# Optimization experiments

Measured on AMD Instinct MI355X. Metric: run time of the kernel, lower is better.

Reference implementation:

```python
import jax, jax.numpy as jnp
import numpy as np

VOCAB = 400000
DIM = 300
NUM_QUERIES = 512
TOP_K = 5


def setup_inputs() -> dict:
    key = jax.random.key(0)
    k1, k2 = jax.random.split(key)
    embedding = jax.random.normal(k1, (VOCAB, DIM), dtype=jnp.float32)
    word_ids = jax.random.randint(k2, (NUM_QUERIES,), 0, VOCAB, dtype=jnp.int64)
    return {"embedding": embedding, "word_ids": word_ids, "k": TOP_K}


def reference(embedding, word_ids, k):
    # Row-normalize the table (done in Synonym.__init__: emb / emb.norm(dim=1, keepdim=True))
    E = embedding / jnp.linalg.norm(embedding, axis=1, keepdims=True)  # [V, d]
    # Per-word GEMV against the full table, batched over queries:
    # torch.mm(word_embedding.view(1,-1), embedding.t()) per word -> [Q, V]
    q = E[word_ids]                      # [Q, d] gather of query word vectors
    sims = jnp.einsum('qd,vd->qv', q, E)  # [Q, V] cosine similarities
    # topk(k, largest=True); the torch code sorts results by value afterwards,
    # lax.top_k already returns values in descending order.
    top_vals, top_ids = jax.lax.top_k(sims, k)  # [Q, k], [Q, k]
    return top_vals, top_ids
```

## Files before the change

### kernel.cpp

```cpp
#include <hip/hip_runtime.h>


#define VOCAB   400000
#define DIM     300
#define NQ      512
#define NT      25000
#define TILE_U  5120
#define QSTR    328
#define QFSTR   304
#define TOPK    5
#define NCAND   3072

using f32x4 = __attribute__((ext_vector_type(4))) float;
using s16x8 = __attribute__((ext_vector_type(8))) short;

__device__ __forceinline__ unsigned short f2bf(float f) {
  unsigned int u = __builtin_bit_cast(unsigned int, f);
  u += 0x7fffu + ((u >> 16) & 1u);
  return (unsigned short)(u >> 16);
}

__device__ __forceinline__ void ins3(float v, int id, float* tv, int* ti) {
  if (v > tv[2]) {
    if (v > tv[0]) {
      tv[2] = tv[1]; ti[2] = ti[1]; tv[1] = tv[0]; ti[1] = ti[0];
      tv[0] = v; ti[0] = id;
    } else if (v > tv[1]) {
      tv[2] = tv[1]; ti[2] = ti[1]; tv[1] = v; ti[1] = id;
    } else {
      tv[2] = v; ti[2] = id;
    }
  }
}

__global__ __launch_bounds__(64)
void qprep_kernel(const float* __restrict__ emb, const int* __restrict__ wid,
                  float* __restrict__ qf, unsigned short* __restrict__ qn) {
  const int q = blockIdx.x;
  const int lane = threadIdx.x;
  const long long w = (long long)wid[q];
  const float* row = emb + w * DIM;
  float x[5];
  double ss = 0.0;
#pragma unroll
  for (int j = 0; j < 5; ++j) {
    const int k = lane + 64 * j;
    x[j] = (k < DIM) ? row[k] : 0.0f;
    ss += (double)x[j] * (double)x[j];
  }
#pragma unroll
  for (int m = 1; m < 64; m <<= 1) ss += __shfl_xor(ss, m, 64);
  const double rinv = 1.0 / sqrt(ss);
#pragma unroll
  for (int j = 0; j < 5; ++j) {
    const int k = lane + 64 * j;
    if (k < DIM) {
      const float v = (float)((double)x[j] * rinv);
      qf[q * QFSTR + k] = v;
      qn[q * QSTR + k] = f2bf(v);
    }
  }
  if (lane < QSTR - DIM) qn[q * QSTR + DIM + lane] = 0;
}

__global__ __launch_bounds__(256)
void prenorm_kernel(const float* __restrict__ emb, unsigned short* __restrict__ sw) {
  const int wave = threadIdx.x >> 6, lane = threadIdx.x & 63;
  const int t = blockIdx.x * 4 + wave;
  const int r = lane & 15, grp = lane >> 4;
  const float* row = emb + (size_t)(t * 16 + r) * DIM;

  float x[10][8];
  float ss = 0.f;
#pragma unroll
  for (int ks = 0; ks < 10; ++ks) {
    const int k0 = ks * 32 + grp * 8;
    if (k0 + 8 <= DIM) {
      const f32x4 u = *(const f32x4*)(row + k0);
      const f32x4 v = *(const f32x4*)(row + k0 + 4);
#pragma unroll
      for (int j = 0; j < 4; ++j) { x[ks][j] = u[j]; x[ks][j + 4] = v[j]; }
    } else {
#pragma unroll
      for (int j = 0; j < 8; ++j) {
        const int k = k0 + j;
        x[ks][j] = (k < DIM) ? row[k] : 0.0f;
      }
    }
#pragma unroll
    for (int j = 0; j < 8; ++j) ss += x[ks][j] * x[ks][j];
  }
  ss += __shfl_xor(ss, 16, 64);
  ss += __shfl_xor(ss, 32, 64);
  const float rinv = rsqrtf(ss);

  unsigned short* dst = sw + (size_t)t * TILE_U + lane * 8;
#pragma unroll
  for (int ks = 0; ks < 10; ++ks) {
    uint4 pk;
    unsigned int w0 = f2bf(x[ks][0] * rinv) | ((unsigned int)f2bf(x[ks][1] * rinv) << 16);
    unsigned int w1 = f2bf(x[ks][2] * rinv) | ((unsigned int)f2bf(x[ks][3] * rinv) << 16);
    unsigned int w2 = f2bf(x[ks][4] * rinv) | ((unsigned int)f2bf(x[ks][5] * rinv) << 16);
    unsigned int w3 = f2bf(x[ks][6] * rinv) | ((unsigned int)f2bf(x[ks][7] * rinv) << 16);
    pk.x = w0; pk.y = w1; pk.z = w2; pk.w = w3;
    *(uint4*)(dst + ks * 512) = pk;
  }
}

__global__ __launch_bounds__(512, 2)
void score_kernel(const unsigned short* __restrict__ sw,
                  const unsigned short* __restrict__ qn,
                  float2* __restrict__ cand) {
  __shared__ __align__(16) unsigned short qlds[128 * QSTR];

  const int tid = threadIdx.x;
  const int wave = tid >> 6, lane = tid & 63;
  const int l15 = lane & 15, grp = lane >> 4;
  const int mtile = blockIdx.x & 3, rb = blockIdx.x >> 2;
  const int rowgrp = wave >> 1, qhalf = wave & 1;

  {
    const uint4* src = (const uint4*)(qn + (size_t)mtile * 128 * QSTR);
    uint4* dst = (uint4*)qlds;
    for (int i = tid; i < 128 * QSTR * 2 / 16; i += 512) dst[i] = src[i];
  }
  __syncthreads();

  float v3[4][3]; int i3[4][3];
#pragma unroll
  for (int qi = 0; qi < 4; ++qi)
#pragma unroll
    for (int j = 0; j < 3; ++j) { v3[qi][j] = -1e30f; i3[qi][j] = 0; }

  const s16x8 zz = {0, 0, 0, 0, 0, 0, 0, 0};
  const int qrow0 = qhalf * 64;

  for (int it = 0; it < 25; ++it) {
    const int tbase = it * 1024 + rb * 16 + rowgrp * 4;
    bool tv[4];
    const unsigned short* ap[4];
#pragma unroll
    for (int vi = 0; vi < 4; ++vi) {
      const int t = tbase + vi;
      tv[vi] = (t < NT);
      ap[vi] = sw + (size_t)(tv[vi] ? t : 0) * TILE_U + lane * 8;
    }

    f32x4 acc[4][4];
#pragma unroll
    for (int qi = 0; qi < 4; ++qi)
#pragma unroll
      for (int vi = 0; vi < 4; ++vi) acc[qi][vi] = {0.f, 0.f, 0.f, 0.f};

#pragma unroll
    for (int ks = 0; ks < 10; ++ks) {
      s16x8 a[4];
#pragma unroll
      for (int vi = 0; vi < 4; ++vi)
        a[vi] = tv[vi] ? *(const s16x8*)(ap[vi] + ks * 512) : zz;
      const unsigned short* bb = qlds + ks * 32 + grp * 8;
#pragma unroll
      for (int qi = 0; qi < 4; ++qi) {
        const s16x8 b = *(const s16x8*)(bb + (qrow0 + qi * 16 + l15) * QSTR);
#pragma unroll
        for (int vi = 0; vi < 4; ++vi)
          acc[qi][vi] = __builtin_amdgcn_mfma_f32_16x16x32_bf16(a[vi], b, acc[qi][vi], 0, 0, 0);
      }
    }

#pragma unroll
    for (int vi = 0; vi < 4; ++vi) {
      if (!tv[vi]) continue;
      const int rbase = (tbase + vi) * 16 + grp * 4;
#pragma unroll
      for (int qi = 0; qi < 4; ++qi) {
#pragma unroll
        for (int rr = 0; rr < 4; ++rr) {
          ins3(acc[qi][vi][rr], rbase + rr, &v3[qi][0], &i3[qi][0]);
        }
      }
    }
  }

  const int slotbase = rb * 48 + rowgrp * 12 + grp * 3;
#pragma unroll
  for (int qi = 0; qi < 4; ++qi) {
    const int q = mtile * 128 + qhalf * 64 + qi * 16 + l15;
    float2* dst = cand + (size_t)q * NCAND + slotbase;
#pragma unroll
    for (int j = 0; j < 3; ++j) {
      float2 e; e.x = v3[qi][j]; e.y = __int_as_float(i3[qi][j]);
      dst[j] = e;
    }
  }
}

__global__ __launch_bounds__(256)
void topk_kernel(const float* __restrict__ emb, const float* __restrict__ qf,
                 const float2* __restrict__ cand, float* __restrict__ out) {
  __shared__ float pV[256 * 6];
  __shared__ int   pI[256 * 6];
  __shared__ int   selI[32];
  __shared__ float resV[32];

  const int q = blockIdx.x;
  const int t = threadIdx.x;
  const float2* cq = cand + (size_t)q * NCAND;

  float bv[6]; int bi[6];
#pragma unroll
  for (int j = 0; j < 6; ++j) { bv[j] = -1e30f; bi[j] = -1; }
  for (int i = t; i < NCAND; i += 256) {
    const float2 e = cq[i];
    const float v = e.x;
    if (v > bv[5]) {
      bv[5] = v; bi[5] = __float_as_int(e.y);
#pragma unroll
      for (int j = 5; j > 0; --j) {
        if (bv[j] > bv[j - 1]) {
          const float tv2 = bv[j]; bv[j] = bv[j - 1]; bv[j - 1] = tv2;
          const int ti2 = bi[j]; bi[j] = bi[j - 1]; bi[j - 1] = ti2;
        }
      }
    }
  }
#pragma unroll
  for (int j = 0; j < 6; ++j) { pV[t * 6 + j] = bv[j]; pI[t * 6 + j] = bi[j]; }
  __syncthreads();

  if (t < 64) {
    for (int r = 0; r < 32; ++r) {
      float mv = -2e30f; int mp = 0;
      for (int i = t; i < 256 * 6; i += 64) {
        const float v = pV[i];
        if (v > mv) { mv = v; mp = i; }
      }
#pragma unroll
      for (int m = 1; m < 64; m <<= 1) {
        const float ov = __shfl_xor(mv, m, 64);
        const int   op = __shfl_xor(mp, m, 64);
        if (ov > mv) { mv = ov; mp = op; }
      }
      if (t == 0) { selI[r] = pI[mp]; pV[mp] = -2e30f; }
      __builtin_amdgcn_wave_barrier();
    }
  }
  __syncthreads();

  {
    const int j = t >> 3, sub = t & 7;
    const int id = selI[j];
    float dot = 0.f, sq = 0.f;
    if (id >= 0) {
      const f32x4* e4 = (const f32x4*)(emb + (size_t)id * DIM);
      const f32x4* q4 = (const f32x4*)(qf + (size_t)q * QFSTR);
      for (int f = sub; f < DIM / 4; f += 8) {
        const f32x4 ev = e4[f], qv = q4[f];
        dot += ev[0]*qv[0] + ev[1]*qv[1] + ev[2]*qv[2] + ev[3]*qv[3];
        sq  += ev[0]*ev[0] + ev[1]*ev[1] + ev[2]*ev[2] + ev[3]*ev[3];
      }
    }
#pragma unroll
    for (int m = 1; m < 8; m <<= 1) {
      dot += __shfl_xor(dot, m, 64);
      sq  += __shfl_xor(sq, m, 64);
    }
    if (sub == 0)
      resV[j] = (id >= 0 && sq > 0.f) ? (float)((double)dot / sqrt((double)sq)) : -2e30f;
  }
  __syncthreads();

  if (t == 0) {
#pragma unroll
    for (int r = 0; r < TOPK; ++r) {
      float mv = -3e30f; int mp = 0;
      for (int i = 0; i < 32; ++i) if (resV[i] > mv) { mv = resV[i]; mp = i; }
      out[q * TOPK + r] = mv;
      out[NQ * TOPK + q * TOPK + r] = (float)selI[mp];
      resV[mp] = -3e30f;
    }
  }
}

extern "C" void kernel_launch(void* const* d_in, const int* in_sizes, int n_in,
                              void* d_out, int out_size, void* d_ws, size_t ws_size,
                              hipStream_t stream) {
  (void)in_sizes; (void)n_in; (void)out_size; (void)ws_size;
  const float* emb = (const float*)d_in[0];
  const int* wid = (const int*)d_in[1];
  float* out = (float*)d_out;

  char* ws = (char*)d_ws;
  unsigned short* qn = (unsigned short*)ws;
  float*  qf   = (float*)(ws + 335872);
  float2* cand = (float2*)(ws + 958464);
  unsigned short* sw = (unsigned short*)(ws + 13541376);

  qprep_kernel<<<NQ, 64, 0, stream>>>(emb, wid, qf, qn);
  prenorm_kernel<<<NT / 4, 256, 0, stream>>>(emb, sw);
  score_kernel<<<256, 512, 0, stream>>>(sw, qn, cand);
  topk_kernel<<<NQ, 256, 0, stream>>>(emb, qf, cand, out);
}
```

Baseline: 1.088 ms.

## Restructure score kernel tiling with pre-swizzled query layout and early-skip top-3

Queries are now written by qprep in the same MFMA-swizzled bf16 tile layout as the table, so the score kernel loads B fragments from LDS with a conflict-free contiguous pattern. The score grid becomes 1024 blocks of 256 threads, each covering 64 queries, with smaller LDS and higher occupancy, and per-wave iteration counts that drop the bounds checks. The top-3 update is skipped when the max of four accumulator values cannot enter the list. A cross-lane shuffle merge reduces the four row-group lists to six candidates per wave. The cost is that the table stream is re-read by 8 query groups instead of 4, which doubles L2/HBM traffic for the embedding tiles.

```diff
diff --git a/kernel.cpp b/kernel.cpp
--- a/kernel.cpp
+++ b/kernel.cpp
@@ -6,7 +6,6 @@
 #define NQ      512
 #define NT      25000
 #define TILE_U  5120
-#define QSTR    328
 #define QFSTR   304
 #define TOPK    5
 #define NCAND   3072
@@ -35,7 +34,7 @@
 
 __global__ __launch_bounds__(64)
 void qprep_kernel(const float* __restrict__ emb, const int* __restrict__ wid,
-                  float* __restrict__ qf, unsigned short* __restrict__ qn) {
+                  float* __restrict__ qf, unsigned short* __restrict__ qsw) {
   const int q = blockIdx.x;
   const int lane = threadIdx.x;
   const long long w = (long long)wid[q];
@@ -54,13 +53,23 @@
 #pragma unroll
   for (int j = 0; j < 5; ++j) {
     const int k = lane + 64 * j;
-    if (k < DIM) {
-      const float v = (float)((double)x[j] * rinv);
-      qf[q * QFSTR + k] = v;
-      qn[q * QSTR + k] = f2bf(v);
-    }
-  }
-  if (lane < QSTR - DIM) qn[q * QSTR + DIM + lane] = 0;
+    if (k < DIM) qf[q * QFSTR + k] = (float)((double)x[j] * rinv);
+  }
+  if (lane < 40) {
+    const int ks = lane >> 2, grp = lane & 3;
+    const int k0 = ks * 32 + grp * 8;
+    unsigned int pw[4];
+#pragma unroll
+    for (int h = 0; h < 4; ++h) {
+      const int k = k0 + 2 * h;
+      float v0 = 0.f, v1 = 0.f;
+      if (k < DIM)     v0 = (float)((double)row[k] * rinv);
+      if (k + 1 < DIM) v1 = (float)((double)row[k + 1] * rinv);
+      pw[h] = (unsigned int)f2bf(v0) | ((unsigned int)f2bf(v1) << 16);
+    }
+    uint4 pk; pk.x = pw[0]; pk.y = pw[1]; pk.z = pw[2]; pk.w = pw[3];
+    *(uint4*)(qsw + (size_t)(q >> 4) * TILE_U + ks * 512 + grp * 128 + (q & 15) * 8) = pk;
+  }
 }
 
 __global__ __launch_bounds__(256)
@@ -107,22 +116,24 @@
   }
 }
 
-__global__ __launch_bounds__(512, 2)
+__global__ __launch_bounds__(256, 4)
 void score_kernel(const unsigned short* __restrict__ sw,
-                  const unsigned short* __restrict__ qn,
+                  const unsigned short* __restrict__ qsw,
                   float2* __restrict__ cand) {
-  __shared__ __align__(16) unsigned short qlds[128 * QSTR];
+  __shared__ __align__(16) unsigned short qlds[4 * TILE_U];
 
   const int tid = threadIdx.x;
   const int wave = tid >> 6, lane = tid & 63;
   const int l15 = lane & 15, grp = lane >> 4;
-  const int mtile = blockIdx.x & 3, rb = blockIdx.x >> 2;
-  const int rowgrp = wave >> 1, qhalf = wave & 1;
+  const int bid = blockIdx.x;
+  const int moct = (bid >> 3) & 7;
+  const int rb = (bid & 7) | ((bid >> 6) << 3);
 
   {
-    const uint4* src = (const uint4*)(qn + (size_t)mtile * 128 * QSTR);
+    const uint4* src = (const uint4*)(qsw + (size_t)moct * 4 * TILE_U);
     uint4* dst = (uint4*)qlds;
-    for (int i = tid; i < 128 * QSTR * 2 / 16; i += 512) dst[i] = src[i];
+#pragma unroll
+    for (int i = 0; i < 10; ++i) dst[tid + 256 * i] = src[tid + 256 * i];
   }
   __syncthreads();
 
@@ -132,19 +143,13 @@
 #pragma unroll
     for (int j = 0; j < 3; ++j) { v3[qi][j] = -1e30f; i3[qi][j] = 0; }
 
-  const s16x8 zz = {0, 0, 0, 0, 0, 0, 0, 0};
-  const int qrow0 = qhalf * 64;
-
-  for (int it = 0; it < 25; ++it) {
-    const int tbase = it * 1024 + rb * 16 + rowgrp * 4;
-    bool tv[4];
-    const unsigned short* ap[4];
-#pragma unroll
-    for (int vi = 0; vi < 4; ++vi) {
-      const int t = tbase + vi;
-      tv[vi] = (t < NT);
-      ap[vi] = sw + (size_t)(tv[vi] ? t : 0) * TILE_U + lane * 8;
-    }
+  const unsigned short* bq = qlds + lane * 8;
+  const int wt = rb * 16 + wave * 4;
+  const int nit = (wt < 424) ? 13 : 12;
+
+  for (int it = 0; it < nit; ++it) {
+    const int t0 = it * 2048 + wt;
+    const unsigned short* ap = sw + (size_t)t0 * TILE_U + lane * 8;
 
     f32x4 acc[4][4];
 #pragma unroll
@@ -157,11 +162,10 @@
       s16x8 a[4];
 #pragma unroll
       for (int vi = 0; vi < 4; ++vi)
-        a[vi] = tv[vi] ? *(const s16x8*)(ap[vi] + ks * 512) : zz;
-      const unsigned short* bb = qlds + ks * 32 + grp * 8;
+        a[vi] = *(const s16x8*)(ap + (size_t)vi * TILE_U + ks * 512);
 #pragma unroll
       for (int qi = 0; qi < 4; ++qi) {
-        const s16x8 b = *(const s16x8*)(bb + (qrow0 + qi * 16 + l15) * QSTR);
+        const s16x8 b = *(const s16x8*)(bq + qi * TILE_U + ks * 512);
 #pragma unroll
         for (int vi = 0; vi < 4; ++vi)
           acc[qi][vi] = __builtin_amdgcn_mfma_f32_16x16x32_bf16(a[vi], b, acc[qi][vi], 0, 0, 0);
@@ -170,27 +174,43 @@
 
 #pragma unroll
     for (int vi = 0; vi < 4; ++vi) {
-      if (!tv[vi]) continue;
-      const int rbase = (tbase + vi) * 16 + grp * 4;
+      const int rbase = (t0 + vi) * 16 + grp * 4;
 #pragma unroll
       for (int qi = 0; qi < 4; ++qi) {
-#pragma unroll
-        for (int rr = 0; rr < 4; ++rr) {
-          ins3(acc[qi][vi][rr], rbase + rr, &v3[qi][0], &i3[qi][0]);
+        const f32x4 a4 = acc[qi][vi];
+        const float m01 = fmaxf(a4[0], a4[1]);
+        const float m23 = fmaxf(a4[2], a4[3]);
+        if (fmaxf(m01, m23) > v3[qi][2]) {
+#pragma unroll
+          for (int rr = 0; rr < 4; ++rr)
+            ins3(a4[rr], rbase + rr, &v3[qi][0], &i3[qi][0]);
         }
       }
     }
   }
 
-  const int slotbase = rb * 48 + rowgrp * 12 + grp * 3;
 #pragma unroll
   for (int qi = 0; qi < 4; ++qi) {
-    const int q = mtile * 128 + qhalf * 64 + qi * 16 + l15;
-    float2* dst = cand + (size_t)q * NCAND + slotbase;
-#pragma unroll
-    for (int j = 0; j < 3; ++j) {
-      float2 e; e.x = v3[qi][j]; e.y = __int_as_float(i3[qi][j]);
-      dst[j] = e;
+    float m0 = v3[qi][0], m1 = v3[qi][1], m2 = v3[qi][2];
+    int   d0 = i3[qi][0], d1 = i3[qi][1], d2 = i3[qi][2];
+    const int q = moct * 64 + qi * 16 + l15;
+    float2* dst = cand + (size_t)q * NCAND + (rb * 24 + wave * 6);
+#pragma unroll
+    for (int r = 0; r < 6; ++r) {
+      float bv = m0; int bi = d0; int bl = grp;
+      float ov = __shfl_xor(bv, 16, 64);
+      int   oi = __shfl_xor(bi, 16, 64);
+      int   ol = __shfl_xor(bl, 16, 64);
+      if (ov > bv || (ov == bv && ol < bl)) { bv = ov; bi = oi; bl = ol; }
+      ov = __shfl_xor(bv, 32, 64);
+      oi = __shfl_xor(bi, 32, 64);
+      ol = __shfl_xor(bl, 32, 64);
+      if (ov > bv || (ov == bv && ol < bl)) { bv = ov; bi = oi; bl = ol; }
+      if (bl == grp) { m0 = m1; d0 = d1; m1 = m2; d1 = d2; m2 = -1e30f; }
+      if (r == grp || r == grp + 4) {
+        float2 e; e.x = bv; e.y = __int_as_float(bi);
+        dst[r] = e;
+      }
     }
   }
 }
@@ -291,13 +311,13 @@
   float* out = (float*)d_out;
 
   char* ws = (char*)d_ws;
-  unsigned short* qn = (unsigned short*)ws;
-  float*  qf   = (float*)(ws + 335872);
-  float2* cand = (float2*)(ws + 958464);
-  unsigned short* sw = (unsigned short*)(ws + 13541376);
-
-  qprep_kernel<<<NQ, 64, 0, stream>>>(emb, wid, qf, qn);
+  unsigned short* qsw = (unsigned short*)ws;
+  float*  qf   = (float*)(ws + 327680);
+  float2* cand = (float2*)(ws + 950272);
+  unsigned short* sw = (unsigned short*)(ws + 13533184);
+
+  qprep_kernel<<<NQ, 64, 0, stream>>>(emb, wid, qf, qsw);
   prenorm_kernel<<<NT / 4, 256, 0, stream>>>(emb, sw);
-  score_kernel<<<256, 512, 0, stream>>>(sw, qn, cand);
+  score_kernel<<<1024, 256, 0, stream>>>(sw, qsw, cand);
   topk_kernel<<<NQ, 256, 0, stream>>>(emb, qf, cand, out);
 }
```

After: 1.246 ms. +14.5%, slower.
